# Performance work log

Measured on AMD Instinct MI355X. Metric: run time of the kernel, lower is better.

The kernel has to match this reference:

```python
import jax, jax.numpy as jnp
import numpy as np
import math

EMB = 512
HEADS = 8
FM = 56
WS = 7


def _relative_position_index(ws):
    coords = np.stack(np.meshgrid(np.arange(ws), np.arange(ws), indexing='ij')).reshape(2, -1)
    rel = coords[:, :, None] - coords[:, None, :]            # [2, ws^2, ws^2]
    rel = rel.transpose(1, 2, 0)                              # [ws^2, ws^2, 2]
    rel = rel + np.abs(rel.min())                             # shift to >= 0 (adds ws-1)
    rel[:, :, 0] = rel[:, :, 0] * (2 * ws - 1)
    return rel.sum(-1)                                        # [ws^2, ws^2] int

REL_IDX = jnp.asarray(_relative_position_index(WS))


def setup_inputs() -> dict:
    key = jax.random.key(0)
    ks = jax.random.split(key, 8)
    B, L, E = 16, FM * FM, EMB
    scale = 0.02
    return {
        'x': jax.random.normal(ks[0], (B, L, E), dtype=jnp.float32),
        'q_w': jax.random.normal(ks[1], (E, E), dtype=jnp.float32) * scale,
        'q_b': jax.random.normal(ks[2], (E,), dtype=jnp.float32) * scale,
        'k_w': jax.random.normal(ks[3], (E, E), dtype=jnp.float32) * scale,
        'k_b': jax.random.normal(ks[4], (E,), dtype=jnp.float32) * scale,
        'v_w': jax.random.normal(ks[5], (E, E), dtype=jnp.float32) * scale,
        'v_b': jax.random.normal(ks[6], (E,), dtype=jnp.float32) * scale,
        'bias_table': jax.random.normal(ks[7], ((2 * WS - 1) ** 2, HEADS), dtype=jnp.float32) * scale,
    }


def reference(x, q_w, q_b, k_w, k_b, v_w, v_b, bias_table):
    B, L, E = x.shape
    nh, d, ws = HEADS, E // HEADS, WS
    n = ws * ws
    # Faithful to the torch code: reshape (NOT channels-last transpose), then window partition
    xr = x.reshape(B, E, FM, FM)
    w = xr.reshape(B, FM // ws, ws, FM // ws, ws, E)
    w = jnp.transpose(w, (0, 1, 3, 2, 4, 5)).reshape(B, -1, ws, ws, E)  # [B, nW, ws, ws, E]
    nW = w.shape[1]
    # Linear projections (torch Linear: x @ W.T + b)
    q = (w @ q_w.T + q_b).reshape(B, nW, nh, n, d)
    k = (w @ k_w.T + k_b).reshape(B, nW, nh, n, d)
    v = (w @ v_w.T + v_b).reshape(B, nW, nh, n, d)
    # Relative position bias: [nh, n, n]
    bias = bias_table[REL_IDX.reshape(-1)].reshape(n, n, nh).transpose(2, 0, 1)
    scores = jnp.einsum('bwhqd,bwhkd->bwhqk', q, k) / math.sqrt(d)
    scores = scores + bias[None, None]
    attn = jax.nn.softmax(scores, axis=-1)
    out = jnp.einsum('bwhqk,bwhkd->bwhqd', attn, v)
    return out.reshape(B, L, E)
```

## Files before the change

### kernel.cpp

```cpp
#include <hip/hip_runtime.h>

typedef __attribute__((ext_vector_type(8))) short short8;
typedef __attribute__((ext_vector_type(4))) short short4v;
typedef __attribute__((ext_vector_type(4))) float float4v;
typedef __attribute__((ext_vector_type(2))) unsigned int uint2v;
typedef __attribute__((ext_vector_type(8))) __bf16 bf16x8;

#define LDS_PQ 57344
#define LDS_PK 107520
#define LDS_TOTAL 157696

__device__ __forceinline__ unsigned short f2bf(float f) {
  unsigned u = __float_as_uint(f);
  u += 0x7FFFu + ((u >> 16) & 1u);
  return (unsigned short)(u >> 16);
}

__device__ __forceinline__ unsigned cvtpk(float lo, float hi) {
  unsigned r;
  asm("v_cvt_pk_bf16_f32 %0, %1, %2" : "=v"(r) : "v"(lo), "v"(hi));
  return r;
}

__device__ __forceinline__ int pswz(int s) { return ((s ^ (s >> 3)) & 7) << 4; }

__global__ void wconv_kernel(const float* __restrict__ qw, const float* __restrict__ kw,
                             const float* __restrict__ vw, short* __restrict__ out) {
  int idx = blockIdx.x * 256 + threadIdx.x;
  int g = idx >> 15;
  int rem = idx & 32767;
  int lane = rem & 63;
  int n01 = (rem >> 6) & 1;
  int w   = (rem >> 7) & 15;
  int kk  = rem >> 11;
  int o  = w * 32 + n01 * 16 + (lane & 15);
  int k0 = kk * 32 + (lane >> 4) * 8;
  const float* src = (g == 0) ? qw : (g == 1) ? kw : vw;
  const float sc = (g == 0) ? 0.125f : 1.0f;
  const float* p = src + o * 512 + k0;
  float4v v0 = *(const float4v*)(p);
  float4v v1 = *(const float4v*)(p + 4);
  short8 o8;
  o8[0] = (short)f2bf(v0.x * sc); o8[1] = (short)f2bf(v0.y * sc);
  o8[2] = (short)f2bf(v0.z * sc); o8[3] = (short)f2bf(v0.w * sc);
  o8[4] = (short)f2bf(v1.x * sc); o8[5] = (short)f2bf(v1.y * sc);
  o8[6] = (short)f2bf(v1.z * sc); o8[7] = (short)f2bf(v1.w * sc);
  *(short8*)(out + idx * 8) = o8;
}

__global__ void bexp_kernel(const float* __restrict__ btab, float* __restrict__ bexp) {
  int idx = blockIdx.x * 256 + threadIdx.x;
  float v = 0.f;
  if (idx < 21952) {
    int h = idx / 2744;
    int rem = idx - h * 2744;
    int i = rem / 56;
    int j = rem - i * 56;
    if (j < 49) {
      int yi = (i * 37) >> 8, xi = i - yi * 7;
      int yj = (j * 37) >> 8, xj = j - yj * 7;
      int t = (yi - yj + 6) * 13 + (xi - xj + 6);
      v = btab[t * 8 + h];
    }
  }
  bexp[idx] = v;
}

__global__ __launch_bounds__(1024, 4) void wattn_kernel(
    const float* __restrict__ x, const short* __restrict__ wcvt,
    const float* __restrict__ qb, const float* __restrict__ kb, const float* __restrict__ vb,
    const float* __restrict__ bexp, float* __restrict__ out) {
  __shared__ __align__(16) char sm[LDS_TOTAL];
  const int tid  = threadIdx.x;
  const int lane = tid & 63;
  const int wave = tid >> 6;
  const int bwi  = blockIdx.x;
  const int bb   = bwi >> 6, wi = bwi & 63;
  const int l15  = lane & 15;
  const int l4   = lane >> 4;
  const int ig   = l4 * 4;
  const int wcol = wave * 32;
  const int ckof = l4 * 16;
  const int h    = wave & 7;
  const int mh   = wave >> 3;

  {
    const float* xb = x + (size_t)bb * (3136 * 512);
    const int whi = (wi >> 3) * 7, wlo = (wi & 7) * 7;
    for (int idx = tid; idx < 49 * 128; idx += 1024) {
      int t = idx >> 7, c4 = idx & 127;
      int yt = (t * 37) >> 8, xt = t - yt * 7;
      int l = (whi + yt) * 56 + wlo + xt;
      float4v v = *(const float4v*)(xb + l * 512 + c4 * 4);
      uint2v o;
      o.x = cvtpk(v.x, v.y);
      o.y = cvtpk(v.z, v.w);
      int byte = t * 1024 + c4 * 8;
      *(uint2v*)(sm + (byte ^ ((t & 7) << 4))) = o;
    }
  }
  __syncthreads();

  int xbase[4], xsw[4];
#pragma unroll
  for (int mt = 0; mt < 4; ++mt) {
    int row = mt * 16 + l15;
    xbase[mt] = row * 1024;
    xsw[mt]   = (row & 7) << 4;
  }

  const short* wgb0 = wcvt + wave * 1024 + lane * 8;

#define LDWP(P, OFF) __builtin_bit_cast(bf16x8, *(const short8*)((P) + (OFF)))
#define LDX(MT, C) __builtin_bit_cast(bf16x8, *(const short8*)(sm + xbase[MT] + ((C) ^ xsw[MT])))

  {
    const short* wq = wgb0;
    const short* wk = wgb0 + 262144;
    float4v aq[2][4], ak[2][4];
#pragma unroll
    for (int nt = 0; nt < 2; ++nt)
#pragma unroll
      for (int mt = 0; mt < 4; ++mt) { aq[nt][mt] = (float4v)0.f; ak[nt][mt] = (float4v)0.f; }

    bf16x8 uq0 = LDWP(wq, 0), uq1 = LDWP(wq, 512);
    bf16x8 uk0 = LDWP(wk, 0), uk1 = LDWP(wk, 512);

#pragma unroll 1
    for (int kk = 0; kk < 16; ++kk) {
      const int nko = ((kk + 1) & 15) * 16384;
      bf16x8 nq0 = LDWP(wq, nko), nq1 = LDWP(wq, nko + 512);
      bf16x8 nk0 = LDWP(wk, nko), nk1 = LDWP(wk, nko + 512);
      const int c_ = kk * 64 + ckof;
      bf16x8 x0 = LDX(0, c_), x1 = LDX(1, c_), x2 = LDX(2, c_), x3 = LDX(3, c_);
      __builtin_amdgcn_s_setprio(1);
      aq[0][0] = __builtin_amdgcn_mfma_f32_16x16x32_bf16(uq0, x0, aq[0][0], 0, 0, 0);
      aq[1][0] = __builtin_amdgcn_mfma_f32_16x16x32_bf16(uq1, x0, aq[1][0], 0, 0, 0);
      ak[0][0] = __builtin_amdgcn_mfma_f32_16x16x32_bf16(uk0, x0, ak[0][0], 0, 0, 0);
      ak[1][0] = __builtin_amdgcn_mfma_f32_16x16x32_bf16(uk1, x0, ak[1][0], 0, 0, 0);
      aq[0][1] = __builtin_amdgcn_mfma_f32_16x16x32_bf16(uq0, x1, aq[0][1], 0, 0, 0);
      aq[1][1] = __builtin_amdgcn_mfma_f32_16x16x32_bf16(uq1, x1, aq[1][1], 0, 0, 0);
      ak[0][1] = __builtin_amdgcn_mfma_f32_16x16x32_bf16(uk0, x1, ak[0][1], 0, 0, 0);
      ak[1][1] = __builtin_amdgcn_mfma_f32_16x16x32_bf16(uk1, x1, ak[1][1], 0, 0, 0);
      aq[0][2] = __builtin_amdgcn_mfma_f32_16x16x32_bf16(uq0, x2, aq[0][2], 0, 0, 0);
      aq[1][2] = __builtin_amdgcn_mfma_f32_16x16x32_bf16(uq1, x2, aq[1][2], 0, 0, 0);
      ak[0][2] = __builtin_amdgcn_mfma_f32_16x16x32_bf16(uk0, x2, ak[0][2], 0, 0, 0);
      ak[1][2] = __builtin_amdgcn_mfma_f32_16x16x32_bf16(uk1, x2, ak[1][2], 0, 0, 0);
      aq[0][3] = __builtin_amdgcn_mfma_f32_16x16x32_bf16(uq0, x3, aq[0][3], 0, 0, 0);
      aq[1][3] = __builtin_amdgcn_mfma_f32_16x16x32_bf16(uq1, x3, aq[1][3], 0, 0, 0);
      ak[0][3] = __builtin_amdgcn_mfma_f32_16x16x32_bf16(uk0, x3, ak[0][3], 0, 0, 0);
      ak[1][3] = __builtin_amdgcn_mfma_f32_16x16x32_bf16(uk1, x3, ak[1][3], 0, 0, 0);
      __builtin_amdgcn_s_setprio(0);
      uq0 = nq0; uq1 = nq1; uk0 = nk0; uk1 = nk1;
    }

#pragma unroll
    for (int nt = 0; nt < 2; ++nt) {
      int o0 = wcol + nt * 16 + ig;
      float4v bq = *(const float4v*)(qb + o0);
      float4v bk = *(const float4v*)(kb + o0);
#pragma unroll
      for (int r = 0; r < 4; ++r) bq[r] *= 0.125f;
      int dd0 = o0 & 63, sg = o0 >> 6;
#pragma unroll
      for (int mt = 0; mt < 4; ++mt) {
        int t = mt * 16 + l15;
        if (t < 49) {
          int s = t * 8 + sg;
          int addr = (s * 128 + dd0 * 2) ^ pswz(s);
          uint2v pq, pk;
          pq.x = cvtpk(aq[nt][mt][0] + bq[0], aq[nt][mt][1] + bq[1]);
          pq.y = cvtpk(aq[nt][mt][2] + bq[2], aq[nt][mt][3] + bq[3]);
          pk.x = cvtpk(ak[nt][mt][0] + bk[0], ak[nt][mt][1] + bk[1]);
          pk.y = cvtpk(ak[nt][mt][2] + bk[2], ak[nt][mt][3] + bk[3]);
          *(uint2v*)(sm + LDS_PQ + addr) = pq;
          *(uint2v*)(sm + LDS_PK + addr) = pk;
        }
      }
    }
  }

  float4v acc[2][4];
  {
    const short* wgb = wgb0 + 2 * 262144;
#pragma unroll
    for (int nt = 0; nt < 2; ++nt)
#pragma unroll
      for (int mt = 0; mt < 4; ++mt) acc[nt][mt] = (float4v)0.f;

    bf16x8 wa0 = LDWP(wgb, 0),     wa1 = LDWP(wgb, 512);
    bf16x8 wb0 = LDWP(wgb, 16384), wb1 = LDWP(wgb, 16384 + 512);
    bf16x8 wc0, wc1, wd0, wd1;

#define GEMM_PHASE(KIDX, W0, W1)                                                          \
    do {                                                                                  \
      const int c_ = (KIDX) * 64 + ckof;                                                  \
      bf16x8 x0_ = LDX(0, c_), x1_ = LDX(1, c_), x2_ = LDX(2, c_), x3_ = LDX(3, c_);      \
      __builtin_amdgcn_s_setprio(1);                                                      \
      acc[0][0] = __builtin_amdgcn_mfma_f32_16x16x32_bf16(W0, x0_, acc[0][0], 0, 0, 0);   \
      acc[1][0] = __builtin_amdgcn_mfma_f32_16x16x32_bf16(W1, x0_, acc[1][0], 0, 0, 0);   \
      acc[0][1] = __builtin_amdgcn_mfma_f32_16x16x32_bf16(W0, x1_, acc[0][1], 0, 0, 0);   \
      acc[1][1] = __builtin_amdgcn_mfma_f32_16x16x32_bf16(W1, x1_, acc[1][1], 0, 0, 0);   \
      acc[0][2] = __builtin_amdgcn_mfma_f32_16x16x32_bf16(W0, x2_, acc[0][2], 0, 0, 0);   \
      acc[1][2] = __builtin_amdgcn_mfma_f32_16x16x32_bf16(W1, x2_, acc[1][2], 0, 0, 0);   \
      acc[0][3] = __builtin_amdgcn_mfma_f32_16x16x32_bf16(W0, x3_, acc[0][3], 0, 0, 0);   \
      acc[1][3] = __builtin_amdgcn_mfma_f32_16x16x32_bf16(W1, x3_, acc[1][3], 0, 0, 0);   \
      __builtin_amdgcn_s_setprio(0);                                                      \
    } while (0)

#pragma unroll 1
    for (int kk = 0; kk < 16; kk += 4) {
      wc0 = LDWP(wgb, ((kk + 2) & 15) * 16384); wc1 = LDWP(wgb, ((kk + 2) & 15) * 16384 + 512);
      GEMM_PHASE(kk, wa0, wa1);
      wd0 = LDWP(wgb, ((kk + 3) & 15) * 16384); wd1 = LDWP(wgb, ((kk + 3) & 15) * 16384 + 512);
      GEMM_PHASE(kk + 1, wb0, wb1);
      wa0 = LDWP(wgb, ((kk + 4) & 15) * 16384); wa1 = LDWP(wgb, ((kk + 4) & 15) * 16384 + 512);
      GEMM_PHASE(kk + 2, wc0, wc1);
      wb0 = LDWP(wgb, ((kk + 5) & 15) * 16384); wb1 = LDWP(wgb, ((kk + 5) & 15) * 16384 + 512);
      GEMM_PHASE(kk + 3, wd0, wd1);
    }
#undef GEMM_PHASE
  }

  __syncthreads();

  float4v scr[4][2];
#pragma unroll
  for (int jt = 0; jt < 4; ++jt)
#pragma unroll
    for (int it = 0; it < 2; ++it) scr[jt][it] = (float4v)0.f;

#pragma unroll
  for (int ks = 0; ks < 2; ++ks) {
    const int dd = ks * 32 + l4 * 8;
    bf16x8 kf[4], qf[2];
#pragma unroll
    for (int jt = 0; jt < 4; ++jt) {
      int s = h * 49 + jt * 16 + l15;
      int flat = s * 128 + dd * 2;
      kf[jt] = __builtin_bit_cast(bf16x8, *(const short8*)(sm + LDS_PK + (flat ^ pswz(s))));
    }
#pragma unroll
    for (int it = 0; it < 2; ++it) {
      int s = h * 49 + (mh * 2 + it) * 16 + l15;
      int flat = s * 128 + dd * 2;
      qf[it] = __builtin_bit_cast(bf16x8, *(const short8*)(sm + LDS_PQ + (flat ^ pswz(s))));
    }
    __builtin_amdgcn_s_setprio(1);
#pragma unroll
    for (int jt = 0; jt < 4; ++jt)
#pragma unroll
      for (int it = 0; it < 2; ++it)
        scr[jt][it] = __builtin_amdgcn_mfma_f32_16x16x32_bf16(kf[jt], qf[it], scr[jt][it], 0, 0, 0);
    __builtin_amdgcn_s_setprio(0);
  }

  {
#pragma unroll
    for (int nt = 0; nt < 2; ++nt) {
      int o0 = wcol + nt * 16 + ig;
      float4v bv = *(const float4v*)(vb + o0);
      int dd0 = o0 & 63, sg = o0 >> 6;
#pragma unroll
      for (int mt = 0; mt < 4; ++mt) {
        int t = mt * 16 + l15;
        if (t < 49) {
          int s = t * 8 + sg;
          int h2 = (s * 1339) >> 16;
          int colb = h2 * 112 + (s - h2 * 49) * 2;
#pragma unroll
          for (int r = 0; r < 4; ++r) {
            int dd = dd0 + r;
            *(unsigned short*)(sm + ((dd * 896 + colb) ^ ((dd & 7) << 4))) =
                f2bf(acc[nt][mt][r] + bv[r]);
          }
        }
      }
    }
    for (int idx = tid; idx < 3584; idx += 1024) {
      int q = idx >> 9;
      int rem = idx & 511;
      int h2 = rem >> 6, dd = rem & 63;
      *(unsigned short*)(sm + ((dd * 896 + h2 * 112 + (49 + q) * 2) ^ ((dd & 7) << 4))) = 0;
    }
  }

  const float* bx = bexp + h * 2744;
#pragma unroll
  for (int it = 0; it < 2; ++it) {
    int i = (mh * 2 + it) * 16 + l15;
    const float* bi = bx + ((i > 48) ? 48 : i) * 56 + ig;
    float mx = -1e30f;
#pragma unroll
    for (int jt = 0; jt < 4; ++jt) {
      float4v b4 = *(const float4v*)(bi + jt * 16);
#pragma unroll
      for (int r = 0; r < 4; ++r) {
        int j = jt * 16 + ig + r;
        float v = (i < 49 && j < 49) ? scr[jt][it][r] + b4[r] : -1e30f;
        scr[jt][it][r] = v;
        mx = fmaxf(mx, v);
      }
    }
    mx = fmaxf(mx, __shfl_xor(mx, 16));
    mx = fmaxf(mx, __shfl_xor(mx, 32));
    float ssum = 0.f;
#pragma unroll
    for (int jt = 0; jt < 4; ++jt)
#pragma unroll
      for (int r = 0; r < 4; ++r) {
        float e = __expf(scr[jt][it][r] - mx);
        scr[jt][it][r] = e;
        ssum += e;
      }
    ssum += __shfl_xor(ssum, 16);
    ssum += __shfl_xor(ssum, 32);
    float inv = 1.f / ssum;
#pragma unroll
    for (int jt = 0; jt < 4; ++jt)
#pragma unroll
      for (int r = 0; r < 4; ++r) scr[jt][it][r] *= inv;
  }

#pragma unroll
  for (int it = 0; it < 2; ++it) {
    int i = (mh * 2 + it) * 16 + l15;
    if (i < 49) {
      int s = h * 49 + i;
      int rowb = s * 128;
      int swz = pswz(s);
#pragma unroll
      for (int jt = 0; jt < 4; ++jt) {
        uint2v pk2;
        pk2.x = cvtpk(scr[jt][it][0], scr[jt][it][1]);
        pk2.y = cvtpk(scr[jt][it][2], scr[jt][it][3]);
        *(uint2v*)(sm + LDS_PQ + ((rowb + jt * 32 + ig * 2) ^ swz)) = pk2;
      }
    }
  }

  __syncthreads();

  float4v oacc[4][2];
#pragma unroll
  for (int dt = 0; dt < 4; ++dt)
#pragma unroll
    for (int tt = 0; tt < 2; ++tt) oacc[dt][tt] = (float4v)0.f;

#pragma unroll
  for (int ks = 0; ks < 2; ++ks) {
    const int tp0 = ks * 32 + l4 * 8;
    bf16x8 vf[4], af[2];
#pragma unroll
    for (int dt = 0; dt < 4; ++dt) {
      int dd = dt * 16 + l15;
      vf[dt] = __builtin_bit_cast(bf16x8,
          *(const short8*)(sm + ((dd * 896 + h * 112 + tp0 * 2) ^ ((dd & 7) << 4))));
    }
#pragma unroll
    for (int tt = 0; tt < 2; ++tt) {
      int t = (mh * 2 + tt) * 16 + l15;
      int tr = (t > 48) ? 48 : t;
      int s = h * 49 + tr;
      af[tt] = __builtin_bit_cast(bf16x8,
          *(const short8*)(sm + LDS_PQ + ((s * 128 + tp0 * 2) ^ pswz(s))));
    }
    __builtin_amdgcn_s_setprio(1);
#pragma unroll
    for (int dt = 0; dt < 4; ++dt)
#pragma unroll
      for (int tt = 0; tt < 2; ++tt)
        oacc[dt][tt] = __builtin_amdgcn_mfma_f32_16x16x32_bf16(vf[dt], af[tt], oacc[dt][tt], 0, 0, 0);
    __builtin_amdgcn_s_setprio(0);
  }

  float* op = out + (size_t)bwi * 25088 + h * 3136;
#pragma unroll
  for (int tt = 0; tt < 2; ++tt) {
    int t = (mh * 2 + tt) * 16 + l15;
    if (t < 49) {
#pragma unroll
      for (int dt = 0; dt < 4; ++dt)
        *(float4v*)(op + t * 64 + dt * 16 + ig) = oacc[dt][tt];
    }
  }
#undef LDWP
#undef LDX
}

extern "C" void kernel_launch(void* const* d_in, const int* in_sizes, int n_in,
                              void* d_out, int out_size, void* d_ws, size_t ws_size,
                              hipStream_t stream) {
  const float* x    = (const float*)d_in[0];
  const float* q_w  = (const float*)d_in[1];
  const float* q_b  = (const float*)d_in[2];
  const float* k_w  = (const float*)d_in[3];
  const float* k_b  = (const float*)d_in[4];
  const float* v_w  = (const float*)d_in[5];
  const float* v_b  = (const float*)d_in[6];
  const float* btab = (const float*)d_in[7];
  short* wcvt = (short*)d_ws;
  float* bexp = (float*)((char*)d_ws + 3 * 262144 * 2);

  hipLaunchKernelGGL(wconv_kernel, dim3(384), dim3(256), 0, stream, q_w, k_w, v_w, wcvt);
  hipLaunchKernelGGL(bexp_kernel, dim3(86), dim3(256), 0, stream, btab, bexp);
  hipLaunchKernelGGL(wattn_kernel, dim3(1024), dim3(1024), 0, stream,
                     x, wcvt, q_b, k_b, v_b, bexp, (float*)d_out);
}
```

Baseline: 147.6 us.

## Split fused window attention into separate QKV projection and attention kernels

Replaces the single fused 1024-thread kernel with two kernels when the workspace is large enough. The first computes the Q, K and V projections per window and writes bf16 Q, K and a transposed V to global memory. The second runs attention with one wave per (window, head), 256-thread blocks and a small LDS footprint. This frees the large LDS and register budget of the fused kernel to raise occupancy, at the cost of about 160 MB of extra global traffic for the intermediate tensors. If the workspace is too small it falls back to the fused kernel.

After: 262.2 us. 1.78x slower.

```diff
diff --git a/kernel.cpp b/kernel.cpp
--- a/kernel.cpp
+++ b/kernel.cpp
@@ -64,6 +64,264 @@
     }
   }
   bexp[idx] = v;
+}
+
+__global__ __launch_bounds__(512, 4) void qkv_kernel(
+    const float* __restrict__ x, const short* __restrict__ wcvt,
+    const float* __restrict__ qb, const float* __restrict__ kb, const float* __restrict__ vb,
+    short* __restrict__ qg, short* __restrict__ kg, short* __restrict__ vg) {
+  __shared__ __align__(16) char sm[50176];
+  const int tid  = threadIdx.x;
+  const int lane = tid & 63;
+  const int wave = tid >> 6;
+  const int bwi  = blockIdx.x;
+  const int bb   = bwi >> 6, wi = bwi & 63;
+  const int l15  = lane & 15;
+  const int l4   = lane >> 4;
+  const int ig   = l4 * 4;
+  const int ckof = l4 * 16;
+
+  {
+    const float* xb = x + (size_t)bb * (3136 * 512);
+    const int whi = (wi >> 3) * 7, wlo = (wi & 7) * 7;
+    for (int idx = tid; idx < 6272; idx += 512) {
+      int t = idx >> 7, c4 = idx & 127;
+      int yt = (t * 37) >> 8, xt = t - yt * 7;
+      int l = (whi + yt) * 56 + wlo + xt;
+      float4v v = *(const float4v*)(xb + l * 512 + c4 * 4);
+      uint2v o;
+      o.x = cvtpk(v.x, v.y);
+      o.y = cvtpk(v.z, v.w);
+      int byte = t * 1024 + c4 * 8;
+      *(uint2v*)(sm + (byte ^ ((t & 7) << 4))) = o;
+    }
+  }
+  __syncthreads();
+
+  const short* wh = wcvt + wave * 2048 + lane * 8;
+
+#pragma unroll 1
+  for (int p = 0; p < 6; ++p) {
+    const int g = p >> 1, mh = p & 1;
+    const short* wgb = wh + g * 262144;
+    const float* bias = (g == 0) ? qb : (g == 1) ? kb : vb;
+    int xb0[2], xs0[2];
+#pragma unroll
+    for (int mt = 0; mt < 2; ++mt) {
+      int row = mh * 32 + mt * 16 + l15;
+      xb0[mt] = row * 1024;
+      xs0[mt] = (row & 7) << 4;
+    }
+    float4v acc[4][2];
+#pragma unroll
+    for (int nt = 0; nt < 4; ++nt)
+#pragma unroll
+      for (int mt = 0; mt < 2; ++mt) acc[nt][mt] = (float4v)0.f;
+
+#pragma unroll 1
+    for (int kk = 0; kk < 16; ++kk) {
+      const short* wp = wgb + kk * 16384;
+      bf16x8 w0 = __builtin_bit_cast(bf16x8, *(const short8*)(wp));
+      bf16x8 w1 = __builtin_bit_cast(bf16x8, *(const short8*)(wp + 512));
+      bf16x8 w2 = __builtin_bit_cast(bf16x8, *(const short8*)(wp + 1024));
+      bf16x8 w3 = __builtin_bit_cast(bf16x8, *(const short8*)(wp + 1536));
+      const int c_ = kk * 64 + ckof;
+      bf16x8 x0 = __builtin_bit_cast(bf16x8, *(const short8*)(sm + xb0[0] + (c_ ^ xs0[0])));
+      bf16x8 x1 = __builtin_bit_cast(bf16x8, *(const short8*)(sm + xb0[1] + (c_ ^ xs0[1])));
+      __builtin_amdgcn_s_setprio(1);
+      acc[0][0] = __builtin_amdgcn_mfma_f32_16x16x32_bf16(w0, x0, acc[0][0], 0, 0, 0);
+      acc[1][0] = __builtin_amdgcn_mfma_f32_16x16x32_bf16(w1, x0, acc[1][0], 0, 0, 0);
+      acc[2][0] = __builtin_amdgcn_mfma_f32_16x16x32_bf16(w2, x0, acc[2][0], 0, 0, 0);
+      acc[3][0] = __builtin_amdgcn_mfma_f32_16x16x32_bf16(w3, x0, acc[3][0], 0, 0, 0);
+      acc[0][1] = __builtin_amdgcn_mfma_f32_16x16x32_bf16(w0, x1, acc[0][1], 0, 0, 0);
+      acc[1][1] = __builtin_amdgcn_mfma_f32_16x16x32_bf16(w1, x1, acc[1][1], 0, 0, 0);
+      acc[2][1] = __builtin_amdgcn_mfma_f32_16x16x32_bf16(w2, x1, acc[2][1], 0, 0, 0);
+      acc[3][1] = __builtin_amdgcn_mfma_f32_16x16x32_bf16(w3, x1, acc[3][1], 0, 0, 0);
+      __builtin_amdgcn_s_setprio(0);
+    }
+
+#pragma unroll
+    for (int nt = 0; nt < 4; ++nt) {
+      int dd0 = nt * 16 + ig;
+      float4v bv = *(const float4v*)(bias + wave * 64 + dd0);
+      if (g == 0) {
+#pragma unroll
+        for (int r = 0; r < 4; ++r) bv[r] *= 0.125f;
+      }
+      if (g < 2) {
+        short* dstbase = ((g == 0) ? qg : kg) +
+                         ((size_t)bwi * 392 + wave) * 64 + dd0;
+#pragma unroll
+        for (int mt = 0; mt < 2; ++mt) {
+          int t = mh * 32 + mt * 16 + l15;
+          if (t < 49) {
+            uint2v p2;
+            p2.x = cvtpk(acc[nt][mt][0] + bv[0], acc[nt][mt][1] + bv[1]);
+            p2.y = cvtpk(acc[nt][mt][2] + bv[2], acc[nt][mt][3] + bv[3]);
+            *(uint2v*)(dstbase + (size_t)t * 512) = p2;
+          }
+        }
+      } else {
+#pragma unroll
+        for (int mt = 0; mt < 2; ++mt) {
+          int t = mh * 32 + mt * 16 + l15;
+          if (t < 49) {
+            int s = t * 8 + wave;
+            int h2 = (s * 1339) >> 16;
+            int tp = s - h2 * 49;
+            short* vp = vg + (size_t)(bwi * 8 + h2) * 3584 + tp;
+#pragma unroll
+            for (int r = 0; r < 4; ++r)
+              vp[(size_t)(dd0 + r) * 56] = (short)f2bf(acc[nt][mt][r] + bv[r]);
+          }
+        }
+      }
+    }
+  }
+
+  {
+    short* vp = vg + (size_t)(bwi * 8 + wave) * 3584 + (size_t)lane * 56;
+#pragma unroll
+    for (int q = 49; q < 56; ++q) vp[q] = 0;
+  }
+  if (bwi == 1023 && tid < 64) vg[(size_t)8192 * 3584 + tid] = 0;
+}
+
+__global__ __launch_bounds__(256, 4) void attn2_kernel(
+    const short* __restrict__ qg, const short* __restrict__ kg, const short* __restrict__ vg,
+    const float* __restrict__ bexp, float* __restrict__ out) {
+  __shared__ __align__(16) char ovs[4][8192];
+  const int tid  = threadIdx.x;
+  const int lane = tid & 63;
+  const int wave = tid >> 6;
+  const int bh   = blockIdx.x * 4 + wave;
+  const int h    = bh & 7, bwi = bh >> 3;
+  const int l15  = lane & 15;
+  const int l4   = lane >> 4;
+  const int ig   = l4 * 4;
+  char* ov = ovs[wave];
+
+  const short* Qh = qg + ((size_t)bwi * 392 + h * 49) * 64;
+  const short* Kh = kg + ((size_t)bwi * 392 + h * 49) * 64;
+  const short* Vh = vg + (size_t)bh * 3584;
+
+  float4v scr[4][4];
+#pragma unroll
+  for (int jt = 0; jt < 4; ++jt)
+#pragma unroll
+    for (int it = 0; it < 4; ++it) scr[jt][it] = (float4v)0.f;
+
+#pragma unroll
+  for (int ks = 0; ks < 2; ++ks) {
+    const int dd = ks * 32 + l4 * 8;
+    bf16x8 kf[4], qf[4];
+#pragma unroll
+    for (int jt = 0; jt < 4; ++jt)
+      kf[jt] = __builtin_bit_cast(bf16x8, *(const short8*)(Kh + (size_t)(jt * 16 + l15) * 64 + dd));
+#pragma unroll
+    for (int it = 0; it < 4; ++it)
+      qf[it] = __builtin_bit_cast(bf16x8, *(const short8*)(Qh + (size_t)(it * 16 + l15) * 64 + dd));
+    __builtin_amdgcn_s_setprio(1);
+#pragma unroll
+    for (int jt = 0; jt < 4; ++jt)
+#pragma unroll
+      for (int it = 0; it < 4; ++it)
+        scr[jt][it] = __builtin_amdgcn_mfma_f32_16x16x32_bf16(kf[jt], qf[it], scr[jt][it], 0, 0, 0);
+    __builtin_amdgcn_s_setprio(0);
+  }
+
+  const float* bx = bexp + h * 2744;
+#pragma unroll
+  for (int it = 0; it < 4; ++it) {
+    int i = it * 16 + l15;
+    const float* bi = bx + ((i > 48) ? 48 : i) * 56 + ig;
+    float mx = -1e30f;
+#pragma unroll
+    for (int jt = 0; jt < 4; ++jt) {
+      float4v b4 = *(const float4v*)(bi + jt * 16);
+#pragma unroll
+      for (int r = 0; r < 4; ++r) {
+        int j = jt * 16 + ig + r;
+        float v = (i < 49 && j < 49) ? scr[jt][it][r] + b4[r] : -1e30f;
+        scr[jt][it][r] = v;
+        mx = fmaxf(mx, v);
+      }
+    }
+    mx = fmaxf(mx, __shfl_xor(mx, 16));
+    mx = fmaxf(mx, __shfl_xor(mx, 32));
+    float ssum = 0.f;
+#pragma unroll
+    for (int jt = 0; jt < 4; ++jt)
+#pragma unroll
+      for (int r = 0; r < 4; ++r) {
+        float e = __expf(scr[jt][it][r] - mx);
+        scr[jt][it][r] = e;
+        ssum += e;
+      }
+    ssum += __shfl_xor(ssum, 16);
+    ssum += __shfl_xor(ssum, 32);
+    float inv = 1.f / ssum;
+#pragma unroll
+    for (int jt = 0; jt < 4; ++jt)
+#pragma unroll
+      for (int r = 0; r < 4; ++r) scr[jt][it][r] *= inv;
+  }
+
+#pragma unroll
+  for (int it = 0; it < 4; ++it) {
+    int i = it * 16 + l15;
+    if (i < 49) {
+      int rowb = i * 128, swz = (i & 7) << 4;
+#pragma unroll
+      for (int jt = 0; jt < 4; ++jt) {
+        uint2v p2;
+        p2.x = cvtpk(scr[jt][it][0], scr[jt][it][1]);
+        p2.y = cvtpk(scr[jt][it][2], scr[jt][it][3]);
+        *(uint2v*)(ov + ((rowb + jt * 32 + ig * 2) ^ swz)) = p2;
+      }
+    }
+  }
+  __syncthreads();
+
+  float4v oacc[4][4];
+#pragma unroll
+  for (int dt = 0; dt < 4; ++dt)
+#pragma unroll
+    for (int tt = 0; tt < 4; ++tt) oacc[dt][tt] = (float4v)0.f;
+
+#pragma unroll
+  for (int ks = 0; ks < 2; ++ks) {
+    const int tp0 = ks * 32 + l4 * 8;
+    bf16x8 vf[4], af[4];
+#pragma unroll
+    for (int dt = 0; dt < 4; ++dt)
+      vf[dt] = __builtin_bit_cast(bf16x8, *(const short8*)(Vh + (size_t)(dt * 16 + l15) * 56 + tp0));
+#pragma unroll
+    for (int tt = 0; tt < 4; ++tt) {
+      int t = tt * 16 + l15;
+      int tr = (t > 48) ? 48 : t;
+      af[tt] = __builtin_bit_cast(bf16x8,
+          *(const short8*)(ov + ((tr * 128 + tp0 * 2) ^ ((tr & 7) << 4))));
+    }
+    __builtin_amdgcn_s_setprio(1);
+#pragma unroll
+    for (int dt = 0; dt < 4; ++dt)
+#pragma unroll
+      for (int tt = 0; tt < 4; ++tt)
+        oacc[dt][tt] = __builtin_amdgcn_mfma_f32_16x16x32_bf16(vf[dt], af[tt], oacc[dt][tt], 0, 0, 0);
+    __builtin_amdgcn_s_setprio(0);
+  }
+
+  float* op = out + (size_t)bwi * 25088 + h * 3136;
+#pragma unroll
+  for (int tt = 0; tt < 4; ++tt) {
+    int t = tt * 16 + l15;
+    if (t < 49) {
+#pragma unroll
+      for (int dt = 0; dt < 4; ++dt)
+        *(float4v*)(op + t * 64 + dt * 16 + ig) = oacc[dt][tt];
+    }
+  }
 }
 
 __global__ __launch_bounds__(1024, 4) void wattn_kernel(
@@ -404,6 +662,21 @@
 
   hipLaunchKernelGGL(wconv_kernel, dim3(384), dim3(256), 0, stream, q_w, k_w, v_w, wcvt);
   hipLaunchKernelGGL(bexp_kernel, dim3(86), dim3(256), 0, stream, btab, bexp);
-  hipLaunchKernelGGL(wattn_kernel, dim3(1024), dim3(1024), 0, stream,
-                     x, wcvt, q_b, k_b, v_b, bexp, (float*)d_out);
-}
+
+  const size_t QG_OFF = 2097152;
+  const size_t KG_OFF = QG_OFF + 51380224 + 4096;
+  const size_t VG_OFF = KG_OFF + 51380224 + 4096;
+  const size_t REQUIRED = VG_OFF + 58720256 + 4096;
+  if (ws_size >= REQUIRED) {
+    short* qg = (short*)((char*)d_ws + QG_OFF);
+    short* kg = (short*)((char*)d_ws + KG_OFF);
+    short* vg = (short*)((char*)d_ws + VG_OFF);
+    hipLaunchKernelGGL(qkv_kernel, dim3(1024), dim3(512), 0, stream,
+                       x, wcvt, q_b, k_b, v_b, qg, kg, vg);
+    hipLaunchKernelGGL(attn2_kernel, dim3(2048), dim3(256), 0, stream,
+                       qg, kg, vg, bexp, (float*)d_out);
+  } else {
+    hipLaunchKernelGGL(wattn_kernel, dim3(1024), dim3(1024), 0, stream,
+                       x, wcvt, q_b, k_b, v_b, bexp, (float*)d_out);
+  }
+}
```
